# Kernel optimization log

Hardware: AMD Instinct MI355X
Metric: run time of the kernel (lower is better)

Reference implementation:

```python
import jax, jax.numpy as jnp
import numpy as np

N, E = 50000, 800000
IN, HID, H1, H2, OUT = 128, 64, 4, 6, 121
NEG_SLOPE = 0.2


def setup_inputs() -> dict:
    key = jax.random.key(0)
    ks = jax.random.split(key, 16)
    s = 0.1  # weight init scale
    return {
        "x": jax.random.normal(ks[0], (N, IN), jnp.float32),
        "src": jax.random.randint(ks[1], (E,), 0, N),
        "dst": jax.random.randint(ks[2], (E,), 0, N),
        # conv1: in=IN, heads=H1, out=HID, concat
        "W1": jax.random.normal(ks[3], (IN, H1 * HID), jnp.float32) * s,
        "a1_src": jax.random.normal(ks[4], (H1, HID), jnp.float32) * s,
        "a1_dst": jax.random.normal(ks[5], (H1, HID), jnp.float32) * s,
        "b1": jnp.zeros((H1 * HID,), jnp.float32),
        # conv2: in=H1*HID, heads=H1, out=HID, concat, residual
        "W2": jax.random.normal(ks[6], (H1 * HID, H1 * HID), jnp.float32) * s,
        "a2_src": jax.random.normal(ks[7], (H1, HID), jnp.float32) * s,
        "a2_dst": jax.random.normal(ks[8], (H1, HID), jnp.float32) * s,
        "b2": jnp.zeros((H1 * HID,), jnp.float32),
        "Wres2": jax.random.normal(ks[9], (H1 * HID, H1 * HID), jnp.float32) * s,
        # conv3: in=H1*HID, heads=H2, out=OUT, mean (concat=False)
        "W3": jax.random.normal(ks[10], (H1 * HID, H2 * OUT), jnp.float32) * s,
        "a3_src": jax.random.normal(ks[11], (H2, OUT), jnp.float32) * s,
        "a3_dst": jax.random.normal(ks[12], (H2, OUT), jnp.float32) * s,
        "b3": jnp.zeros((OUT,), jnp.float32),
    }


def _segment_softmax(e, seg, n):
    # e: [E, H], softmax over edges sharing the same destination node
    m = jax.ops.segment_max(e, seg, num_segments=n)
    ex = jnp.exp(e - m[seg])
    s = jax.ops.segment_sum(ex, seg, num_segments=n)
    return ex / (s[seg] + 1e-16)


def _gat_conv(x, src, dst, W, a_src, a_dst, b, heads, ch, concat, Wres=None):
    n = x.shape[0]
    h = (x @ W).reshape(n, heads, ch)                       # [N, H, C]
    al_s = jnp.sum(h * a_src, axis=-1)                      # [N, H]
    al_d = jnp.sum(h * a_dst, axis=-1)                      # [N, H]
    e = jax.nn.leaky_relu(al_s[src] + al_d[dst], NEG_SLOPE)  # [E, H]
    alpha = _segment_softmax(e, dst, n)                     # [E, H]
    msg = h[src] * alpha[..., None]                         # [E, H, C]
    out = jax.ops.segment_sum(msg, dst, num_segments=n)     # [N, H, C]
    out = out.reshape(n, heads * ch) if concat else out.mean(axis=1)
    if Wres is not None:
        out = out + x @ Wres
    return out + b


def reference(x, src, dst, W1, a1_src, a1_dst, b1, W2, a2_src, a2_dst, b2,
              Wres2, W3, a3_src, a3_dst, b3):
    n = x.shape[0]
    # PyG GATConv default: add self-loops
    loop = jnp.arange(n, dtype=src.dtype)
    s = jnp.concatenate([src, loop])
    d = jnp.concatenate([dst, loop])
    h = jax.nn.elu(_gat_conv(x, s, d, W1, a1_src, a1_dst, b1, H1, HID, True))
    h = jax.nn.elu(_gat_conv(h, s, d, W2, a2_src, a2_dst, b2, H1, HID, True, Wres=Wres2))
    h = _gat_conv(h, s, d, W3, a3_src, a3_dst, b3, H2, OUT, False)
    return jax.nn.sigmoid(h)
```

## Files before the change

kernel.cpp:

```cpp
#include <hip/hip_runtime.h>
#include <hip/hip_bf16.h>


#define NODES 50000
#define EDGES 800000
#define MPAD  50048
#define C0    25088
#define C1R   24960

typedef unsigned short u16;
typedef __attribute__((ext_vector_type(8))) short bf16x8;
typedef __attribute__((ext_vector_type(4))) float f32x4;

__device__ __forceinline__ float bf16f(u16 r) {
    return __uint_as_float(((unsigned)r) << 16);
}
__device__ __forceinline__ u16 f2b(float v) {
    __hip_bfloat16 b = __float2bfloat16(v);
    return *(u16*)&b;
}
__device__ __forceinline__ float blo(unsigned d) { return __uint_as_float(d << 16); }
__device__ __forceinline__ float bhi(unsigned d) { return __uint_as_float(d & 0xffff0000u); }


__global__ void fill_ones_kernel(int* __restrict__ deg, int n) {
    int i = blockIdx.x * blockDim.x + threadIdx.x;
    if (i < n) deg[i] = 1;
}

__global__ void hist_kernel(const int* __restrict__ dst, int* __restrict__ deg, int E) {
    int e = blockIdx.x * blockDim.x + threadIdx.x;
    if (e < E) atomicAdd(&deg[dst[e]], 1);
}

__global__ void deg_bsum_kernel(const int* __restrict__ deg, int* __restrict__ bsum, int n) {
    int tid = threadIdx.x, lane = tid & 63, wid = tid >> 6;
    int i = blockIdx.x * 256 + tid;
    int v = (i < n) ? deg[i] : 0;
    #pragma unroll
    for (int ofs = 32; ofs > 0; ofs >>= 1) v += __shfl_down(v, ofs);
    __shared__ int sp[4];
    if (lane == 0) sp[wid] = v;
    __syncthreads();
    if (tid == 0) bsum[blockIdx.x] = sp[0] + sp[1] + sp[2] + sp[3];
}

__global__ void bsum_scan_kernel(int* __restrict__ bsum, int* __restrict__ row_ptr,
                                 int nb, int n) {
    int tid = threadIdx.x, lane = tid & 63, wid = tid >> 6;
    int v = (tid < nb) ? bsum[tid] : 0;
    int incl = v;
    #pragma unroll
    for (int ofs = 1; ofs < 64; ofs <<= 1) {
        int t = __shfl_up(incl, ofs);
        if (lane >= ofs) incl += t;
    }
    __shared__ int sp[4];
    if (lane == 63) sp[wid] = incl;
    __syncthreads();
    int add = 0;
    for (int k = 0; k < wid; k++) add += sp[k];
    int excl = incl - v + add;
    if (tid < nb) bsum[tid] = excl;
    if (tid == nb - 1) row_ptr[n] = excl + v;
}

__global__ void deg_scan_kernel(const int* __restrict__ deg, const int* __restrict__ bofs,
                                int* __restrict__ row_ptr, int* __restrict__ cursor, int n) {
    int tid = threadIdx.x, lane = tid & 63, wid = tid >> 6;
    int i = blockIdx.x * 256 + tid;
    int v = (i < n) ? deg[i] : 0;
    int incl = v;
    #pragma unroll
    for (int ofs = 1; ofs < 64; ofs <<= 1) {
        int t = __shfl_up(incl, ofs);
        if (lane >= ofs) incl += t;
    }
    __shared__ int sp[4];
    if (lane == 63) sp[wid] = incl;
    __syncthreads();
    int add = bofs[blockIdx.x];
    for (int k = 0; k < wid; k++) add += sp[k];
    int excl = incl - v + add;
    if (i < n) { row_ptr[i] = excl; cursor[i] = excl; }
}

__global__ void scatter_kernel(const int* __restrict__ src, const int* __restrict__ dst,
                               int E, int n, int* __restrict__ cursor, int* __restrict__ csr_src) {
    int e = blockIdx.x * blockDim.x + threadIdx.x;
    if (e < E) {
        int d = dst[e];
        int p = atomicAdd(&cursor[d], 1);
        csr_src[p] = src[e];
    } else if (e < E + n) {
        int i = e - E;
        int p = atomicAdd(&cursor[i], 1);
        csr_src[p] = i;
    }
}


__global__ void convertA4_kernel(const float* __restrict__ A, u16* __restrict__ O, int total4) {
    int idx = blockIdx.x * blockDim.x + threadIdx.x;
    if (idx >= total4) return;
    float4 f = ((const float4*)A)[idx];
    ushort4 o;
    o.x = f2b(f.x); o.y = f2b(f.y); o.z = f2b(f.z); o.w = f2b(f.w);
    ((ushort4*)O)[idx] = o;
}

__global__ void convertW_kernel(const float* __restrict__ W, int ldw, int col0,
                                int Ncols, int Npad, int K, u16* __restrict__ WT) {
    int idx = blockIdx.x * blockDim.x + threadIdx.x;
    if (idx >= Npad * K) return;
    int k = idx % K;
    int n = idx / K;
    float f = (n < Ncols) ? W[(size_t)k * ldw + col0 + n] : 0.f;
    WT[(size_t)n * K + k] = f2b(f);
}

__global__ void convertW3stack_kernel(const float* __restrict__ W3, u16* __restrict__ WT) {
    int idx = blockIdx.x * blockDim.x + threadIdx.x;
    if (idx >= 128 * 1536) return;
    int q = idx % 1536;
    int n = idx / 1536;
    int h = q >> 8, k = q & 255;
    float f = (n < 121) ? W3[(size_t)k * 726 + h * 121 + n] : 0.f;
    WT[(size_t)n * 1536 + q] = f2b(f);
}

__global__ void prep_cmat_kernel(const float* __restrict__ W3, const float* __restrict__ a3s,
                                 const float* __restrict__ a3d, float* __restrict__ cm) {
    int idx = blockIdx.x * blockDim.x + threadIdx.x;
    if (idx >= 12 * 256) return;
    int k = idx & 255;
    int o = idx >> 8;
    int h = (o < 6) ? o : o - 6;
    const float* a = (o < 6) ? a3s : a3d;
    float v = 0.f;
    for (int c = 0; c < 121; c++) v += W3[(size_t)k * 726 + h * 121 + c] * a[h * 121 + c];
    cm[(size_t)o * 256 + k] = v;
}


__global__ __launch_bounds__(256) void gemm_mfma_kernel(
    const u16* __restrict__ A, const u16* __restrict__ B,
    float* __restrict__ Cf, u16* __restrict__ Cb, u16* __restrict__ Cb2,
    int M, int Ncols, int K2, int ldc, int split,
    const float* __restrict__ bias, int act) {
    __shared__ __align__(16) u16 As[128][40];
    __shared__ __align__(16) u16 Bs[128][40];
    int tid = threadIdx.x;
    int lane = tid & 63;
    int wv = tid >> 6;
    int quad = lane >> 4, lm = lane & 15;
    int wm = (wv & 1) * 64, wn = (wv >> 1) * 64;
    int bm = blockIdx.x * 128, bn = blockIdx.y * 128;

    f32x4 zero = {0.f, 0.f, 0.f, 0.f};
    f32x4 acc[4][4];
    #pragma unroll
    for (int i = 0; i < 4; i++)
        #pragma unroll
        for (int j = 0; j < 4; j++) acc[i][j] = zero;

    for (int k0 = 0; k0 < K2; k0 += 32) {
        #pragma unroll
        for (int it = 0; it < 2; ++it) {
            int chunk = tid + it * 256;
            int row = chunk >> 2, seg = chunk & 3;
            uint4 va = *(const uint4*)(A + (size_t)(bm + row) * K2 + k0 + seg * 8);
            uint4 vb = *(const uint4*)(B + (size_t)(bn + row) * K2 + k0 + seg * 8);
            *(uint4*)&As[row][seg * 8] = va;
            *(uint4*)&Bs[row][seg * 8] = vb;
        }
        __syncthreads();
        bf16x8 af[4], bfr[4];
        #pragma unroll
        for (int i = 0; i < 4; i++) af[i] = *(const bf16x8*)&As[wm + i * 16 + lm][quad * 8];
        #pragma unroll
        for (int j = 0; j < 4; j++) bfr[j] = *(const bf16x8*)&Bs[wn + j * 16 + lm][quad * 8];
        #pragma unroll
        for (int i = 0; i < 4; i++)
            #pragma unroll
            for (int j = 0; j < 4; j++)
                acc[i][j] = __builtin_amdgcn_mfma_f32_16x16x32_bf16(af[i], bfr[j], acc[i][j], 0, 0, 0);
        __syncthreads();
    }

    #pragma unroll
    for (int i = 0; i < 4; i++) {
        #pragma unroll
        for (int j = 0; j < 4; j++) {
            int col = bn + wn + j * 16 + lm;
            if (col >= Ncols) continue;
            int row_base = bm + wm + i * 16 + quad * 4;
            #pragma unroll
            for (int r = 0; r < 4; r++) {
                int row = row_base + r;
                if (row >= M) continue;
                float v = acc[i][j][r];
                if (act == 1) {
                    v += bias[col];
                    v = 1.f / (1.f + __expf(-v));
                    Cf[(size_t)row * ldc + col] = v;
                } else if (col < split) {
                    Cb[(size_t)row * ldc + col] = f2b(v);
                } else {
                    Cb2[(size_t)row * ldc + col - split] = f2b(v);
                }
            }
        }
    }
}


__global__ void row_alpha4_kernel(const u16* __restrict__ f, const float* __restrict__ a_s,
                                  const float* __restrict__ a_d, float* __restrict__ al_s,
                                  float* __restrict__ al_d, int n) {
    int wv = threadIdx.x >> 6, lane = threadIdx.x & 63;
    int i = blockIdx.x * 4 + wv;
    if (i >= n) return;
    ushort4 hv = *(const ushort4*)(f + (size_t)i * 256 + lane * 4);
    float4 as = *(const float4*)(a_s + lane * 4);
    float4 ad = *(const float4*)(a_d + lane * 4);
    float x0 = bf16f(hv.x), x1 = bf16f(hv.y), x2 = bf16f(hv.z), x3 = bf16f(hv.w);
    float ps = x0 * as.x + x1 * as.y + x2 * as.z + x3 * as.w;
    float pd = x0 * ad.x + x1 * ad.y + x2 * ad.z + x3 * ad.w;
    #pragma unroll
    for (int ofs = 1; ofs < 16; ofs <<= 1) {
        ps += __shfl_xor(ps, ofs);
        pd += __shfl_xor(pd, ofs);
    }
    if ((lane & 15) == 0) {
        int hd = lane >> 4;
        al_s[(size_t)i * 4 + hd] = ps;
        al_d[(size_t)i * 4 + hd] = pd;
    }
}

__global__ __launch_bounds__(256) void al3_kernel(const u16* __restrict__ o2b,
                                                  const float* __restrict__ cm,
                                                  float* __restrict__ al3, int n) {
    int wid = threadIdx.x >> 6, lane = threadIdx.x & 63;
    int i = blockIdx.x * 4 + wid;
    if (i >= n) return;
    uint2 d = *(const uint2*)(o2b + (size_t)i * 256 + lane * 4);
    float v0 = blo(d.x), v1 = bhi(d.x), v2 = blo(d.y), v3 = bhi(d.y);
    float a[12];
    #pragma unroll
    for (int o = 0; o < 12; o++) {
        float4 c = *(const float4*)(cm + (size_t)o * 256 + lane * 4);
        a[o] = v0 * c.x + v1 * c.y + v2 * c.z + v3 * c.w;
    }
    #pragma unroll
    for (int ofs = 1; ofs < 64; ofs <<= 1) {
        #pragma unroll
        for (int o = 0; o < 12; o++) a[o] += __shfl_xor(a[o], ofs);
    }
    if (lane == 0) {
        float4* dst = (float4*)(al3 + (size_t)i * 12);
        dst[0] = make_float4(a[0], a[1], a[2], a[3]);
        dst[1] = make_float4(a[4], a[5], a[6], a[7]);
        dst[2] = make_float4(a[8], a[9], a[10], a[11]);
    }
}


__global__ __launch_bounds__(256) void agg4_fused(
    const u16* __restrict__ f, const float* __restrict__ al_s, const float* __restrict__ al_d,
    const int* __restrict__ row_ptr, const int* __restrict__ csr_src,
    const float* __restrict__ bias, const u16* __restrict__ resb,
    u16* __restrict__ outb, int n) {
    int wid = threadIdx.x >> 6, lane = threadIdx.x & 63;
    int i = blockIdx.x * 4 + wid;
    if (i >= n) return;
    int beg = row_ptr[i], end = row_ptr[i + 1];
    int h_st = lane >> 4;
    int el = lane & 15;
    int half = lane >> 5;
    int c8 = (lane & 31) * 8;
    float ald_st = al_d[(size_t)i * 4 + h_st];
    float acc[8] = {};
    float S = 0.f;
    for (int base = beg; base < end; base += 16) {
        int cnt = min(16, end - base);
        int idxv = csr_src[base + min(el, cnt - 1)];
        float av = al_s[(size_t)idxv * 4 + h_st] + ald_st;
        av = av > 0.f ? av : 0.2f * av;
        float ex = __expf(fminf(av, 60.f));
        for (int e = 0; e < cnt; e += 2) {
            int ei = e + half;
            int eu = ei < cnt ? ei : e;
            int s = __shfl(idxv, eu);
            float w = __shfl(ex, ((lane & 24) << 1) | eu);
            if (ei >= cnt) w = 0.f;
            S += w;
            uint4 d = *(const uint4*)(f + (size_t)s * 256 + c8);
            acc[0] = fmaf(w, blo(d.x), acc[0]); acc[1] = fmaf(w, bhi(d.x), acc[1]);
            acc[2] = fmaf(w, blo(d.y), acc[2]); acc[3] = fmaf(w, bhi(d.y), acc[3]);
            acc[4] = fmaf(w, blo(d.z), acc[4]); acc[5] = fmaf(w, bhi(d.z), acc[5]);
            acc[6] = fmaf(w, blo(d.w), acc[6]); acc[7] = fmaf(w, bhi(d.w), acc[7]);
        }
    }
    #pragma unroll
    for (int k = 0; k < 8; k++) acc[k] += __shfl_xor(acc[k], 32);
    S += __shfl_xor(S, 32);
    if (half == 0) {
        float inv = 1.f / (S + 1e-16f);
        float4 b0 = *(const float4*)(bias + c8);
        float4 b1 = *(const float4*)(bias + c8 + 4);
        float v[8];
        v[0] = acc[0] * inv + b0.x; v[1] = acc[1] * inv + b0.y;
        v[2] = acc[2] * inv + b0.z; v[3] = acc[3] * inv + b0.w;
        v[4] = acc[4] * inv + b1.x; v[5] = acc[5] * inv + b1.y;
        v[6] = acc[6] * inv + b1.z; v[7] = acc[7] * inv + b1.w;
        if (resb) {
            uint4 r = *(const uint4*)(resb + (size_t)i * 256 + c8);
            v[0] += blo(r.x); v[1] += bhi(r.x); v[2] += blo(r.y); v[3] += bhi(r.y);
            v[4] += blo(r.z); v[5] += bhi(r.z); v[6] += blo(r.w); v[7] += bhi(r.w);
        }
        #pragma unroll
        for (int k = 0; k < 8; k++) v[k] = v[k] > 0.f ? v[k] : (__expf(v[k]) - 1.f);
        uint4 o;
        o.x = (unsigned)f2b(v[0]) | ((unsigned)f2b(v[1]) << 16);
        o.y = (unsigned)f2b(v[2]) | ((unsigned)f2b(v[3]) << 16);
        o.z = (unsigned)f2b(v[4]) | ((unsigned)f2b(v[5]) << 16);
        o.w = (unsigned)f2b(v[6]) | ((unsigned)f2b(v[7]) << 16);
        *(uint4*)(outb + (size_t)i * 256 + c8) = o;
    }
}


__global__ __launch_bounds__(256) void aggS_fused(
    const u16* __restrict__ x, const float* __restrict__ al3,
    const int* __restrict__ row_ptr, const int* __restrict__ csr_src,
    u16* __restrict__ S, int node0, int count) {
    __shared__ int s_i[4][16];
    __shared__ float s_w[4][96];
    int wid = threadIdx.x >> 6, lane = threadIdx.x & 63;
    int li = blockIdx.x * 4 + wid;
    if (li >= count) return;
    int i = node0 + li;
    int beg = row_ptr[i], end = row_ptr[i + 1];
    int c4 = lane * 4;
    int e16 = lane & 15;
    int hA = lane >> 4;
    int hB = 4 + (lane >> 4);
    float aldA = al3[(size_t)i * 12 + 6 + hA];
    float aldB = (lane < 32) ? al3[(size_t)i * 12 + 6 + hB] : 0.f;
    float acc[6][4] = {};
    float Ssum[6] = {};
    for (int base = beg; base < end; base += 16) {
        int cnt = min(16, end - base);
        int idxe = csr_src[base + min(e16, cnt - 1)];
        if (lane < 16) s_i[wid][lane] = idxe;
        float vA = al3[(size_t)idxe * 12 + hA] + aldA;
        vA = vA > 0.f ? vA : 0.2f * vA;
        float exA = __expf(fminf(vA, 60.f));
        if (e16 < cnt) s_w[wid][e16 * 6 + hA] = exA;
        if (lane < 32) {
            float vB = al3[(size_t)idxe * 12 + hB] + aldB;
            vB = vB > 0.f ? vB : 0.2f * vB;
            float exB = __expf(fminf(vB, 60.f));
            if (e16 < cnt) s_w[wid][e16 * 6 + hB] = exB;
        }
        for (int e = 0; e < cnt; e++) {
            int s = s_i[wid][e];
            uint2 d = *(const uint2*)(x + (size_t)s * 256 + c4);
            float v0 = blo(d.x), v1 = bhi(d.x), v2 = blo(d.y), v3 = bhi(d.y);
            #pragma unroll
            for (int hh = 0; hh < 6; hh++) {
                float w = s_w[wid][e * 6 + hh];
                Ssum[hh] += w;
                acc[hh][0] = fmaf(w, v0, acc[hh][0]);
                acc[hh][1] = fmaf(w, v1, acc[hh][1]);
                acc[hh][2] = fmaf(w, v2, acc[hh][2]);
                acc[hh][3] = fmaf(w, v3, acc[hh][3]);
            }
        }
    }
    #pragma unroll
    for (int hh = 0; hh < 6; hh++) {
        float inv = 1.f / (6.f * (Ssum[hh] + 1e-16f));
        ushort4 o;
        o.x = f2b(acc[hh][0] * inv);
        o.y = f2b(acc[hh][1] * inv);
        o.z = f2b(acc[hh][2] * inv);
        o.w = f2b(acc[hh][3] * inv);
        *(ushort4*)(S + (size_t)li * 1536 + hh * 256 + c4) = o;
    }
}


extern "C" void kernel_launch(void* const* d_in, const int* in_sizes, int n_in,
                              void* d_out, int out_size, void* d_ws, size_t ws_size,
                              hipStream_t stream) {
    const float* x      = (const float*)d_in[0];
    const int*   src    = (const int*)d_in[1];
    const int*   dst    = (const int*)d_in[2];
    const float* W1     = (const float*)d_in[3];
    const float* a1_src = (const float*)d_in[4];
    const float* a1_dst = (const float*)d_in[5];
    const float* b1     = (const float*)d_in[6];
    const float* W2     = (const float*)d_in[7];
    const float* a2_src = (const float*)d_in[8];
    const float* a2_dst = (const float*)d_in[9];
    const float* b2     = (const float*)d_in[10];
    const float* Wres2  = (const float*)d_in[11];
    const float* W3     = (const float*)d_in[12];
    const float* a3_src = (const float*)d_in[13];
    const float* a3_dst = (const float*)d_in[14];
    const float* b3     = (const float*)d_in[15];
    float* out = (float*)d_out;

    const int N = NODES, E = EDGES;
    const int EN = E + N;
    const int NB = (N + 255) / 256;

    char* p = (char*)d_ws;
    auto alloc = [&](size_t bytes) -> char* {
        char* r = p;
        p += (bytes + 511) & ~(size_t)511;
        return r;
    };
    int*   row_ptr = (int*)alloc((size_t)(N + 1) * sizeof(int));
    int*   cursor  = (int*)alloc((size_t)N * sizeof(int));
    int*   deg     = (int*)alloc((size_t)N * sizeof(int));
    int*   bsum    = (int*)alloc(256 * sizeof(int));
    int*   csr_src = (int*)alloc((size_t)EN * sizeof(int));
    float* al      = (float*)alloc((size_t)N * 12 * sizeof(float));
    float* cm      = (float*)alloc((size_t)12 * 256 * sizeof(float));
    u16*   o2b     = (u16*)alloc((size_t)MPAD * 256 * sizeof(u16));
    u16*   WT2     = (u16*)alloc((size_t)512 * 256 * sizeof(u16));
    u16*   W3sT    = (u16*)alloc((size_t)128 * 1536 * sizeof(u16));
    const size_t A2B_B  = (size_t)MPAD * 256 * sizeof(u16);
    const size_t F1B_B  = (size_t)N * 256 * sizeof(u16);
    const size_t RESB_B = (size_t)N * 256 * sizeof(u16);
    const size_t S_B    = (size_t)C0 * 1536 * sizeof(u16);
    size_t r2_bytes = A2B_B + F1B_B + RESB_B;
    if (S_B > r2_bytes) r2_bytes = S_B;
    char* r2 = alloc(r2_bytes + 1024);
    u16* A2b  = (u16*)r2;
    u16* f1b  = (u16*)(r2 + A2B_B);
    u16* resb = (u16*)(r2 + A2B_B + F1B_B);
    u16* A2a  = (u16*)(r2 + A2B_B + F1B_B);
    u16* Sb   = (u16*)r2;
    (void)ws_size; (void)n_in; (void)in_sizes; (void)out_size;

    float* al_s = al;
    float* al_d = al + (size_t)4 * N;

    fill_ones_kernel<<<NB, 256, 0, stream>>>(deg, N);
    hist_kernel<<<(E + 255) / 256, 256, 0, stream>>>(dst, deg, E);
    deg_bsum_kernel<<<NB, 256, 0, stream>>>(deg, bsum, N);
    bsum_scan_kernel<<<1, 256, 0, stream>>>(bsum, row_ptr, NB, N);
    deg_scan_kernel<<<NB, 256, 0, stream>>>(deg, bsum, row_ptr, cursor, N);
    scatter_kernel<<<(E + N + 255) / 256, 256, 0, stream>>>(src, dst, E, N, cursor, csr_src);

    int nwb = (N + 3) / 4;

    convertA4_kernel<<<(N * 128 / 4 + 255) / 256, 256, 0, stream>>>(x, A2a, N * 128 / 4);
    convertW_kernel<<<(256 * 128 + 255) / 256, 256, 0, stream>>>(W1, 256, 0, 256, 256, 128, WT2);
    {
        dim3 g(MPAD / 128, 2);
        gemm_mfma_kernel<<<g, 256, 0, stream>>>(A2a, WT2, nullptr, f1b, nullptr,
                                                N, 256, 128, 256, 9999, nullptr, 0);
    }
    row_alpha4_kernel<<<nwb, 256, 0, stream>>>(f1b, a1_src, a1_dst, al_s, al_d, N);
    agg4_fused<<<nwb, 256, 0, stream>>>(f1b, al_s, al_d, row_ptr, csr_src, b1, nullptr, A2b, N);

    convertW_kernel<<<(256 * 256 + 255) / 256, 256, 0, stream>>>(W2, 256, 0, 256, 256, 256, WT2);
    convertW_kernel<<<(256 * 256 + 255) / 256, 256, 0, stream>>>(Wres2, 256, 0, 256, 256, 256,
                                                                 WT2 + (size_t)256 * 256);
    {
        dim3 g(MPAD / 128, 4);
        gemm_mfma_kernel<<<g, 256, 0, stream>>>(A2b, WT2, nullptr, f1b, resb,
                                                N, 512, 256, 256, 256, nullptr, 0);
    }
    row_alpha4_kernel<<<nwb, 256, 0, stream>>>(f1b, a2_src, a2_dst, al_s, al_d, N);
    agg4_fused<<<nwb, 256, 0, stream>>>(f1b, al_s, al_d, row_ptr, csr_src, b2, resb, o2b, N);

    prep_cmat_kernel<<<(12 * 256 + 255) / 256, 256, 0, stream>>>(W3, a3_src, a3_dst, cm);
    al3_kernel<<<nwb, 256, 0, stream>>>(o2b, cm, al, N);
    convertW3stack_kernel<<<(128 * 1536 + 255) / 256, 256, 0, stream>>>(W3, W3sT);
    {
        aggS_fused<<<(C0 + 3) / 4, 256, 0, stream>>>(o2b, al, row_ptr, csr_src, Sb, 0, C0);
        dim3 g0(C0 / 128, 1);
        gemm_mfma_kernel<<<g0, 256, 0, stream>>>(Sb, W3sT, out, nullptr, nullptr,
                                                 C0, 121, 1536, 121, 9999, b3, 1);
        aggS_fused<<<(N - C0 + 3) / 4, 256, 0, stream>>>(o2b, al, row_ptr, csr_src, Sb, C0, N - C0);
        dim3 g1(C1R / 128, 1);
        gemm_mfma_kernel<<<g1, 256, 0, stream>>>(Sb, W3sT, out + (size_t)C0 * 121, nullptr, nullptr,
                                                 N - C0, 121, 1536, 121, 9999, b3, 1);
    }
}
```

Baseline: 688.3 us.

## Use skinny 32-row MFMA GEMM for layer 3 and widen aggS loads

Replaces the general 128x128-tile MFMA GEMM for the final 1536-K, 121-column projection with a dedicated skinny kernel. It uses 32-row blocks and shared-memory B only, with A fragments loaded directly from global, so far more blocks run than the previous single-column grid of 128-row tiles. The layer-3 aggregation kernel now has each half-wave process a different edge with 8-wide uint4 loads, then combines the halves with cross-lane shuffles. This doubles edge-level parallelism per wave and widens memory transactions, at the cost of more registers for the 6x8 accumulators. The generic GEMM loses its sigmoid/bias path, and the second chunk size is redefined.

```diff
diff --git a/kernel.cpp b/kernel.cpp
--- a/kernel.cpp
+++ b/kernel.cpp
@@ -6,7 +6,7 @@
 #define EDGES 800000
 #define MPAD  50048
 #define C0    25088
-#define C1R   24960
+#define C1    24912
 
 typedef unsigned short u16;
 typedef __attribute__((ext_vector_type(8))) short bf16x8;
@@ -145,9 +145,8 @@
 
 __global__ __launch_bounds__(256) void gemm_mfma_kernel(
     const u16* __restrict__ A, const u16* __restrict__ B,
-    float* __restrict__ Cf, u16* __restrict__ Cb, u16* __restrict__ Cb2,
-    int M, int Ncols, int K2, int ldc, int split,
-    const float* __restrict__ bias, int act) {
+    u16* __restrict__ Cb, u16* __restrict__ Cb2,
+    int M, int Ncols, int K2, int ldc, int split) {
     __shared__ __align__(16) u16 As[128][40];
     __shared__ __align__(16) u16 Bs[128][40];
     int tid = threadIdx.x;
@@ -200,16 +199,61 @@
                 int row = row_base + r;
                 if (row >= M) continue;
                 float v = acc[i][j][r];
-                if (act == 1) {
-                    v += bias[col];
-                    v = 1.f / (1.f + __expf(-v));
-                    Cf[(size_t)row * ldc + col] = v;
-                } else if (col < split) {
-                    Cb[(size_t)row * ldc + col] = f2b(v);
-                } else {
-                    Cb2[(size_t)row * ldc + col - split] = f2b(v);
-                }
+                if (col < split) Cb[(size_t)row * ldc + col] = f2b(v);
+                else             Cb2[(size_t)row * ldc + col - split] = f2b(v);
             }
+        }
+    }
+}
+
+
+__global__ __launch_bounds__(256) void gemm_skinny(
+    const u16* __restrict__ A, const u16* __restrict__ B,
+    float* __restrict__ C, const float* __restrict__ bias, int count) {
+    __shared__ __align__(16) u16 Bs[128][40];
+    int tid = threadIdx.x, lane = tid & 63, wv = tid >> 6;
+    int quad = lane >> 4, lm = lane & 15;
+    int bm = blockIdx.x * 32;
+    int mrow = (wv >> 1) * 16;
+    int ncol = (wv & 1) * 64;
+    int arow = bm + mrow + lm;
+    if (arow >= count) arow = count - 1;
+    const u16* Ap = A + (size_t)arow * 1536;
+
+    f32x4 zero = {0.f, 0.f, 0.f, 0.f};
+    f32x4 acc[4];
+    #pragma unroll
+    for (int j = 0; j < 4; j++) acc[j] = zero;
+
+    for (int k0 = 0; k0 < 1536; k0 += 32) {
+        #pragma unroll
+        for (int it = 0; it < 2; ++it) {
+            int chunk = tid + it * 256;
+            int r = chunk >> 2, s = chunk & 3;
+            *(uint4*)&Bs[r][s * 8] = *(const uint4*)(B + (size_t)r * 1536 + k0 + s * 8);
+        }
+        bf16x8 af = *(const bf16x8*)(Ap + k0 + quad * 8);
+        __syncthreads();
+        #pragma unroll
+        for (int j = 0; j < 4; j++) {
+            bf16x8 bf = *(const bf16x8*)&Bs[ncol + j * 16 + lm][quad * 8];
+            acc[j] = __builtin_amdgcn_mfma_f32_16x16x32_bf16(af, bf, acc[j], 0, 0, 0);
+        }
+        __syncthreads();
+    }
+
+    #pragma unroll
+    for (int j = 0; j < 4; j++) {
+        int col = ncol + j * 16 + lm;
+        if (col >= 121) continue;
+        int row_base = bm + mrow + quad * 4;
+        #pragma unroll
+        for (int r = 0; r < 4; r++) {
+            int row = row_base + r;
+            if (row >= count) continue;
+            float v = acc[j][r] + bias[col];
+            v = 1.f / (1.f + __expf(-v));
+            C[(size_t)row * 121 + col] = v;
         }
     }
 }
@@ -343,13 +387,14 @@
     if (li >= count) return;
     int i = node0 + li;
     int beg = row_ptr[i], end = row_ptr[i + 1];
-    int c4 = lane * 4;
+    int half = lane >> 5;
+    int c8 = (lane & 31) * 8;
     int e16 = lane & 15;
     int hA = lane >> 4;
     int hB = 4 + (lane >> 4);
     float aldA = al3[(size_t)i * 12 + 6 + hA];
     float aldB = (lane < 32) ? al3[(size_t)i * 12 + 6 + hB] : 0.f;
-    float acc[6][4] = {};
+    float acc[6][8] = {};
     float Ssum[6] = {};
     for (int base = beg; base < end; base += 16) {
         int cnt = min(16, end - base);
@@ -365,30 +410,46 @@
             float exB = __expf(fminf(vB, 60.f));
             if (e16 < cnt) s_w[wid][e16 * 6 + hB] = exB;
         }
-        for (int e = 0; e < cnt; e++) {
-            int s = s_i[wid][e];
-            uint2 d = *(const uint2*)(x + (size_t)s * 256 + c4);
+        for (int e = 0; e < cnt; e += 2) {
+            int ei = e + half;
+            bool valid = ei < cnt;
+            int eu = valid ? ei : e;
+            int s = s_i[wid][eu];
+            uint4 d = *(const uint4*)(x + (size_t)s * 256 + c8);
             float v0 = blo(d.x), v1 = bhi(d.x), v2 = blo(d.y), v3 = bhi(d.y);
+            float v4 = blo(d.z), v5 = bhi(d.z), v6 = blo(d.w), v7 = bhi(d.w);
             #pragma unroll
             for (int hh = 0; hh < 6; hh++) {
-                float w = s_w[wid][e * 6 + hh];
+                float w = valid ? s_w[wid][eu * 6 + hh] : 0.f;
                 Ssum[hh] += w;
                 acc[hh][0] = fmaf(w, v0, acc[hh][0]);
                 acc[hh][1] = fmaf(w, v1, acc[hh][1]);
                 acc[hh][2] = fmaf(w, v2, acc[hh][2]);
                 acc[hh][3] = fmaf(w, v3, acc[hh][3]);
+                acc[hh][4] = fmaf(w, v4, acc[hh][4]);
+                acc[hh][5] = fmaf(w, v5, acc[hh][5]);
+                acc[hh][6] = fmaf(w, v6, acc[hh][6]);
+                acc[hh][7] = fmaf(w, v7, acc[hh][7]);
             }
         }
     }
     #pragma unroll
     for (int hh = 0; hh < 6; hh++) {
-        float inv = 1.f / (6.f * (Ssum[hh] + 1e-16f));
-        ushort4 o;
-        o.x = f2b(acc[hh][0] * inv);
-        o.y = f2b(acc[hh][1] * inv);
-        o.z = f2b(acc[hh][2] * inv);
-        o.w = f2b(acc[hh][3] * inv);
-        *(ushort4*)(S + (size_t)li * 1536 + hh * 256 + c4) = o;
+        Ssum[hh] += __shfl_xor(Ssum[hh], 32);
+        #pragma unroll
+        for (int k = 0; k < 8; k++) acc[hh][k] += __shfl_xor(acc[hh][k], 32);
+    }
+    if (half == 0) {
+        #pragma unroll
+        for (int hh = 0; hh < 6; hh++) {
+            float inv = 1.f / (6.f * (Ssum[hh] + 1e-16f));
+            uint4 o;
+            o.x = (unsigned)f2b(acc[hh][0] * inv) | ((unsigned)f2b(acc[hh][1] * inv) << 16);
+            o.y = (unsigned)f2b(acc[hh][2] * inv) | ((unsigned)f2b(acc[hh][3] * inv) << 16);
+            o.z = (unsigned)f2b(acc[hh][4] * inv) | ((unsigned)f2b(acc[hh][5] * inv) << 16);
+            o.w = (unsigned)f2b(acc[hh][6] * inv) | ((unsigned)f2b(acc[hh][7] * inv) << 16);
+            *(uint4*)(S + (size_t)li * 1536 + hh * 256 + c8) = o;
+        }
     }
 }
 
@@ -464,8 +525,7 @@
     convertW_kernel<<<(256 * 128 + 255) / 256, 256, 0, stream>>>(W1, 256, 0, 256, 256, 128, WT2);
     {
         dim3 g(MPAD / 128, 2);
-        gemm_mfma_kernel<<<g, 256, 0, stream>>>(A2a, WT2, nullptr, f1b, nullptr,
-                                                N, 256, 128, 256, 9999, nullptr, 0);
+        gemm_mfma_kernel<<<g, 256, 0, stream>>>(A2a, WT2, f1b, nullptr, N, 256, 128, 256, 9999);
     }
     row_alpha4_kernel<<<nwb, 256, 0, stream>>>(f1b, a1_src, a1_dst, al_s, al_d, N);
     agg4_fused<<<nwb, 256, 0, stream>>>(f1b, al_s, al_d, row_ptr, csr_src, b1, nullptr, A2b, N);
@@ -475,8 +535,7 @@
                                                                  WT2 + (size_t)256 * 256);
     {
         dim3 g(MPAD / 128, 4);
-        gemm_mfma_kernel<<<g, 256, 0, stream>>>(A2b, WT2, nullptr, f1b, resb,
-                                                N, 512, 256, 256, 256, nullptr, 0);
+        gemm_mfma_kernel<<<g, 256, 0, stream>>>(A2b, WT2, f1b, resb, N, 512, 256, 256, 256);
     }
     row_alpha4_kernel<<<nwb, 256, 0, stream>>>(f1b, a2_src, a2_dst, al_s, al_d, N);
     agg4_fused<<<nwb, 256, 0, stream>>>(f1b, al_s, al_d, row_ptr, csr_src, b2, resb, o2b, N);
@@ -486,12 +545,8 @@
     convertW3stack_kernel<<<(128 * 1536 + 255) / 256, 256, 0, stream>>>(W3, W3sT);
     {
         aggS_fused<<<(C0 + 3) / 4, 256, 0, stream>>>(o2b, al, row_ptr, csr_src, Sb, 0, C0);
-        dim3 g0(C0 / 128, 1);
-        gemm_mfma_kernel<<<g0, 256, 0, stream>>>(Sb, W3sT, out, nullptr, nullptr,
-                                                 C0, 121, 1536, 121, 9999, b3, 1);
-        aggS_fused<<<(N - C0 + 3) / 4, 256, 0, stream>>>(o2b, al, row_ptr, csr_src, Sb, C0, N - C0);
-        dim3 g1(C1R / 128, 1);
-        gemm_mfma_kernel<<<g1, 256, 0, stream>>>(Sb, W3sT, out + (size_t)C0 * 121, nullptr, nullptr,
-                                                 N - C0, 121, 1536, 121, 9999, b3, 1);
-    }
-}
+        gemm_skinny<<<(C0 + 31) / 32, 256, 0, stream>>>(Sb, W3sT, out, b3, C0);
+        aggS_fused<<<(C1 + 3) / 4, 256, 0, stream>>>(o2b, al, row_ptr, csr_src, Sb, C0, C1);
+        gemm_skinny<<<(C1 + 31) / 32, 256, 0, stream>>>(Sb, W3sT, out + (size_t)C0 * 121, b3, C1);
+    }
+}
```

Measured after the change: 701.5 us. No clear change (+1.9%).
